# Kernel tuning notes

Hardware: AMD Instinct MI355X
Metric: run time of the kernel (lower is better)

## Reference

```python
import jax, jax.numpy as jnp
import numpy as np

LEAKY_SLOPE = 0.2

def gcn_conv(x, W, b, src, dst, deg_inv_sqrt, num_nodes):
    # GCNConv: out = D^{-1/2} (A+I) D^{-1/2} X W + b
    h = x @ W                                   # [N, out]
    norm = deg_inv_sqrt[src] * deg_inv_sqrt[dst]  # [E']
    msg = h[src] * norm[:, None]                # gather + scale
    out = jax.ops.segment_sum(msg, dst, num_segments=num_nodes)
    return out + b

def gcn_forward(x, edge_index, W1, b1, W2, b2, W3, b3):
    num_nodes = x.shape[0]
    loop = jnp.arange(num_nodes, dtype=edge_index.dtype)
    src = jnp.concatenate([edge_index[0], loop])  # add self-loops
    dst = jnp.concatenate([edge_index[1], loop])
    deg = jax.ops.segment_sum(jnp.ones_like(dst, dtype=x.dtype), dst,
                              num_segments=num_nodes)
    deg_inv_sqrt = jnp.where(deg > 0, jax.lax.rsqrt(deg), 0.0)
    # dropout is identity in eval mode (training=False)
    h = gcn_conv(x, W1, b1, src, dst, deg_inv_sqrt, num_nodes)
    h = jax.nn.leaky_relu(h, negative_slope=LEAKY_SLOPE)
    h = gcn_conv(h, W2, b2, src, dst, deg_inv_sqrt, num_nodes)
    h = jax.nn.leaky_relu(h, negative_slope=LEAKY_SLOPE)
    h = gcn_conv(h, W3, b3, src, dst, deg_inv_sqrt, num_nodes)
    return h

def setup_inputs() -> dict:
    key = jax.random.key(0)
    ks = jax.random.split(key, 8)
    N, F, E, C = 100000, 256, 3200000, 40
    x = jax.random.normal(ks[0], (N, F), dtype=jnp.float32)
    edge_index = jax.random.randint(ks[1], (2, E), 0, N, dtype=jnp.int64)
    W1 = jax.random.normal(ks[2], (F, 128), dtype=jnp.float32) * (1.0 / np.sqrt(F))
    b1 = jnp.zeros((128,), dtype=jnp.float32)
    W2 = jax.random.normal(ks[3], (128, 16), dtype=jnp.float32) * (1.0 / np.sqrt(128))
    b2 = jnp.zeros((16,), dtype=jnp.float32)
    W3 = jax.random.normal(ks[4], (16, C), dtype=jnp.float32) * (1.0 / np.sqrt(16))
    b3 = jnp.zeros((C,), dtype=jnp.float32)
    return {"x": x, "edge_index": edge_index, "W1": W1, "b1": b1,
            "W2": W2, "b2": b2, "W3": W3, "b3": b3}

def reference(x, edge_index, W1, b1, W2, b2, W3, b3):
    return gcn_forward(x, edge_index, W1, b1, W2, b2, W3, b3)
```

## Files before the change

### kernel.cpp

```cpp
#include <hip/hip_runtime.h>
#include <hip/hip_fp16.h>
#include <math.h>

#define LEAKY 0.2f
#define BP 6
#define BSZ 64
#define NBUK_MAX 2048

typedef _Float16 f16x8 __attribute__((ext_vector_type(8)));
typedef float f32x4 __attribute__((ext_vector_type(4)));

union H2 { __half2 h; int i; };
union H8 { __half2 h[4]; float4 f; };

__device__ inline __half2 shfl_xor_h2(__half2 v, int m) {
    H2 u; u.h = v;
    u.i = __shfl_xor(u.i, m);
    return u.h;
}


__global__ __launch_bounds__(256) void khist(const int* __restrict__ dst,
                                             int* __restrict__ bhist,
                                             int E, int nbuk) {
    __shared__ int hist[NBUK_MAX];
    int t = threadIdx.x;
    for (int i = t; i < nbuk; i += 256) hist[i] = 0;
    __syncthreads();
    for (int e = blockIdx.x * 256 + t; e < E; e += gridDim.x * 256)
        atomicAdd(&hist[dst[e] >> BP], 1);
    __syncthreads();
    for (int i = t; i < nbuk; i += 256) {
        int v = hist[i];
        if (v) atomicAdd(&bhist[i], v);
    }
}

__global__ __launch_bounds__(1024) void bscan(const int* __restrict__ bhist,
                                              int* __restrict__ bbase,
                                              int* __restrict__ bcur, int nbuk) {
    __shared__ int s[1024];
    int t = threadIdx.x;
    int v[4]; int sum = 0;
    #pragma unroll
    for (int i = 0; i < 4; ++i) {
        int idx = t * 4 + i;
        v[i] = (idx < nbuk) ? bhist[idx] : 0;
        sum += v[i];
    }
    s[t] = sum; __syncthreads();
    for (int off = 1; off < 1024; off <<= 1) {
        int a = (t >= off) ? s[t - off] : 0;
        __syncthreads();
        s[t] += a;
        __syncthreads();
    }
    int run = (t > 0) ? s[t - 1] : 0;
    #pragma unroll
    for (int i = 0; i < 4; ++i) {
        int idx = t * 4 + i;
        if (idx < nbuk) { bbase[idx] = run; bcur[idx] = run; run += v[i]; }
    }
    if (t == 1023) bbase[nbuk] = s[1023];
}

__global__ __launch_bounds__(256) void kscatter2(const int* __restrict__ src,
                                                 const int* __restrict__ dst,
                                                 int* __restrict__ bcur,
                                                 int* __restrict__ ebuf,
                                                 int E, int nbuk, int chunk) {
    __shared__ int hist[NBUK_MAX];
    int t = threadIdx.x;
    int base = blockIdx.x * chunk;
    int end = min(base + chunk, E);
    for (int i = t; i < nbuk; i += 256) hist[i] = 0;
    __syncthreads();
    for (int e = base + t; e < end; e += 256)
        atomicAdd(&hist[dst[e] >> BP], 1);
    __syncthreads();
    for (int i = t; i < nbuk; i += 256) {
        int c = hist[i];
        hist[i] = c ? atomicAdd(&bcur[i], c) : 0;
    }
    __syncthreads();
    for (int e = base + t; e < end; e += 256) {
        int d = dst[e];
        int pos = atomicAdd(&hist[d >> BP], 1);
        ebuf[pos] = ((d & (BSZ - 1)) << 17) | src[e];
    }
}

__global__ __launch_bounds__(256) void kcount(const int* __restrict__ ebuf,
                                              const int* __restrict__ bbase,
                                              int* __restrict__ cnt,
                                              float* __restrict__ dis, int N) {
    __shared__ int h[BSZ];
    int b = blockIdx.x, t = threadIdx.x;
    if (t < BSZ) h[t] = 0;
    __syncthreads();
    int beg = bbase[b], end = bbase[b + 1];
    for (int j = beg + t; j < end; j += 256)
        atomicAdd(&h[(ebuf[j] >> 17) & (BSZ - 1)], 1);
    __syncthreads();
    if (t < BSZ) {
        int node = b * BSZ + t;
        if (node < N) {
            int c = h[t] + 1;
            cnt[node] = c;
            dis[node] = rsqrtf((float)c);
        }
    }
}

__global__ void scan_block(const int* __restrict__ cnt, int* rowptr, int* bsum, int n) {
    __shared__ int s[256];
    int t = threadIdx.x;
    int i = blockIdx.x * 256 + t;
    int v = (i < n) ? cnt[i] : 0;
    s[t] = v; __syncthreads();
    for (int off = 1; off < 256; off <<= 1) {
        int a = (t >= off) ? s[t - off] : 0;
        __syncthreads();
        s[t] += a;
        __syncthreads();
    }
    if (i < n) rowptr[i] = s[t] - v;
    if (t == 255) bsum[blockIdx.x] = s[255];
}

__global__ void scan_tops(int* bsum, int nb, int* rowptr, int n) {
    __shared__ int s[512];
    int t = threadIdx.x;
    int v = (t < nb) ? bsum[t] : 0;
    s[t] = v; __syncthreads();
    for (int off = 1; off < 512; off <<= 1) {
        int a = (t >= off) ? s[t - off] : 0;
        __syncthreads();
        s[t] += a;
        __syncthreads();
    }
    if (t < nb) bsum[t] = s[t] - v;
    if (t == 511) rowptr[n] = s[511];
}

__global__ void scan_add(int* rowptr, const int* __restrict__ bsum, int n) {
    int i = blockIdx.x * 256 + threadIdx.x;
    if (i < n) rowptr[i] += bsum[blockIdx.x];
}

__global__ __launch_bounds__(256) void kplace(const int* __restrict__ ebuf,
                                              const int* __restrict__ bbase,
                                              const int* __restrict__ rowptr,
                                              int* __restrict__ col, int N) {
    __shared__ int cur[BSZ];
    int b = blockIdx.x, t = threadIdx.x;
    if (t < BSZ) {
        int node = b * BSZ + t;
        if (node < N) {
            int r = rowptr[node];
            col[r] = node;
            cur[t] = r + 1;
        }
    }
    __syncthreads();
    int beg = bbase[b], end = bbase[b + 1];
    for (int j = beg + t; j < end; j += 256) {
        int v = ebuf[j];
        int dl = (v >> 17) & (BSZ - 1);
        int p = atomicAdd(&cur[dl], 1);
        col[p] = v & 0x1FFFF;
    }
}

__global__ __launch_bounds__(256) void wtrans(const float* __restrict__ W1,
                                              const float* __restrict__ W2,
                                              __half* __restrict__ W1t,
                                              __half* __restrict__ W2t) {
    int idx = blockIdx.x * 256 + threadIdx.x;
    if (idx < 32768) {
        int n = idx >> 8, k = idx & 255;
        W1t[idx] = __float2half(W1[k * 128 + n]);
    } else if (idx < 32768 + 2048) {
        int i = idx - 32768;
        int n = i >> 7, k = i & 127;
        W2t[i] = __float2half(W2[k * 16 + n]);
    }
}

__global__ __launch_bounds__(256) void gemm1_mfma(
        const float* __restrict__ x, const __half* __restrict__ W1t,
        const float* __restrict__ dis, __half* __restrict__ C, int M) {
    int wave = threadIdx.x >> 6;
    int lane = threadIdx.x & 63;
    int m = lane & 15, q = lane >> 4;
    int row0 = (blockIdx.x * 4 + wave) * 16;
    int arow = row0 + m;
    bool aval = arow < M;
    const float* xr = x + (size_t)arow * 256 + q * 8;
    f32x4 acc[8];
    #pragma unroll
    for (int c = 0; c < 8; ++c) acc[c] = (f32x4){0.f, 0.f, 0.f, 0.f};
    for (int k0 = 0; k0 < 256; k0 += 32) {
        f16x8 a;
        if (aval) {
            float4 v0 = *(const float4*)(xr + k0);
            float4 v1 = *(const float4*)(xr + k0 + 4);
            a[0] = (_Float16)v0.x; a[1] = (_Float16)v0.y;
            a[2] = (_Float16)v0.z; a[3] = (_Float16)v0.w;
            a[4] = (_Float16)v1.x; a[5] = (_Float16)v1.y;
            a[6] = (_Float16)v1.z; a[7] = (_Float16)v1.w;
        } else {
            #pragma unroll
            for (int i = 0; i < 8; ++i) a[i] = (_Float16)0.f;
        }
        #pragma unroll
        for (int c = 0; c < 8; ++c) {
            f16x8 b = *(const f16x8*)(W1t + (size_t)(c * 16 + m) * 256 + k0 + q * 8);
            acc[c] = __builtin_amdgcn_mfma_f32_16x16x32_f16(a, b, acc[c], 0, 0, 0);
        }
    }
    float dw[4];
    #pragma unroll
    for (int r = 0; r < 4; ++r) {
        int rr = row0 + q * 4 + r;
        dw[r] = (rr < M) ? dis[rr] : 0.f;
    }
    #pragma unroll
    for (int c = 0; c < 8; ++c) {
        #pragma unroll
        for (int r = 0; r < 4; ++r) {
            int rr = row0 + q * 4 + r;
            if (rr < M)
                C[(size_t)rr * 128 + c * 16 + m] = __float2half(acc[c][r] * dw[r]);
        }
    }
}

__global__ __launch_bounds__(256) void gemm2_mfma(
        const __half* __restrict__ A, const __half* __restrict__ W2t,
        const float* __restrict__ dis, __half* __restrict__ C, int M) {
    int wave = threadIdx.x >> 6;
    int lane = threadIdx.x & 63;
    int m = lane & 15, q = lane >> 4;
    int row0 = (blockIdx.x * 4 + wave) * 16;
    int arow = row0 + m;
    bool aval = arow < M;
    const __half* ar = A + (size_t)arow * 128 + q * 8;
    f32x4 acc = (f32x4){0.f, 0.f, 0.f, 0.f};
    #pragma unroll
    for (int k0 = 0; k0 < 128; k0 += 32) {
        f16x8 a;
        if (aval) {
            a = *(const f16x8*)(ar + k0);
        } else {
            #pragma unroll
            for (int i = 0; i < 8; ++i) a[i] = (_Float16)0.f;
        }
        f16x8 b = *(const f16x8*)(W2t + (size_t)m * 128 + k0 + q * 8);
        acc = __builtin_amdgcn_mfma_f32_16x16x32_f16(a, b, acc, 0, 0, 0);
    }
    #pragma unroll
    for (int r = 0; r < 4; ++r) {
        int rr = row0 + q * 4 + r;
        if (rr < M)
            C[(size_t)rr * 16 + m] = __float2half(acc[r] * dis[rr]);
    }
}

__global__ __launch_bounds__(256) void prop128(
        const __half* __restrict__ h, const int* __restrict__ rowptr,
        const int* __restrict__ col, const float* __restrict__ dis,
        const float* __restrict__ bias, __half* __restrict__ out, int N) {
    int n = (blockIdx.x * 256 + threadIdx.x) >> 6;
    if (n >= N) return;
    int lane = threadIdx.x & 63;
    int eo = lane >> 4;
    int q = lane & 15;
    const float4* __restrict__ h4 = (const float4*)h;
    int beg = rowptr[n], end = rowptr[n + 1];
    __half2 acc[4];
    acc[0] = acc[1] = acc[2] = acc[3] = __float2half2_rn(0.f);
    int j = beg + eo;
    for (; j + 12 < end; j += 16) {
        int s0 = col[j], s1 = col[j + 4], s2 = col[j + 8], s3 = col[j + 12];
        H8 u0, u1, u2, u3;
        u0.f = h4[(size_t)s0 * 16 + q];
        u1.f = h4[(size_t)s1 * 16 + q];
        u2.f = h4[(size_t)s2 * 16 + q];
        u3.f = h4[(size_t)s3 * 16 + q];
        #pragma unroll
        for (int i = 0; i < 4; ++i) acc[i] = __hadd2(acc[i], u0.h[i]);
        #pragma unroll
        for (int i = 0; i < 4; ++i) acc[i] = __hadd2(acc[i], u1.h[i]);
        #pragma unroll
        for (int i = 0; i < 4; ++i) acc[i] = __hadd2(acc[i], u2.h[i]);
        #pragma unroll
        for (int i = 0; i < 4; ++i) acc[i] = __hadd2(acc[i], u3.h[i]);
    }
    for (; j + 4 < end; j += 8) {
        int s0 = col[j], s1 = col[j + 4];
        H8 u0, u1;
        u0.f = h4[(size_t)s0 * 16 + q];
        u1.f = h4[(size_t)s1 * 16 + q];
        #pragma unroll
        for (int i = 0; i < 4; ++i) acc[i] = __hadd2(acc[i], u0.h[i]);
        #pragma unroll
        for (int i = 0; i < 4; ++i) acc[i] = __hadd2(acc[i], u1.h[i]);
    }
    for (; j < end; j += 4) {
        int s = col[j];
        H8 u; u.f = h4[(size_t)s * 16 + q];
        #pragma unroll
        for (int i = 0; i < 4; ++i) acc[i] = __hadd2(acc[i], u.h[i]);
    }
    #pragma unroll
    for (int i = 0; i < 4; ++i) {
        acc[i] = __hadd2(acc[i], shfl_xor_h2(acc[i], 16));
        acc[i] = __hadd2(acc[i], shfl_xor_h2(acc[i], 32));
    }
    if (eo == 0) {
        float dn = dis[n];
        const float4* b4 = (const float4*)bias;
        float4 bA = b4[q * 2];
        float4 bB = b4[q * 2 + 1];
        float2 f0 = __half22float2(acc[0]);
        float2 f1 = __half22float2(acc[1]);
        float2 f2 = __half22float2(acc[2]);
        float2 f3 = __half22float2(acc[3]);
        float o0 = fmaf(dn, f0.x, bA.x), o1 = fmaf(dn, f0.y, bA.y);
        float o2 = fmaf(dn, f1.x, bA.z), o3 = fmaf(dn, f1.y, bA.w);
        float o4 = fmaf(dn, f2.x, bB.x), o5 = fmaf(dn, f2.y, bB.y);
        float o6 = fmaf(dn, f3.x, bB.z), o7 = fmaf(dn, f3.y, bB.w);
        o0 = o0 > 0.f ? o0 : LEAKY * o0;  o1 = o1 > 0.f ? o1 : LEAKY * o1;
        o2 = o2 > 0.f ? o2 : LEAKY * o2;  o3 = o3 > 0.f ? o3 : LEAKY * o3;
        o4 = o4 > 0.f ? o4 : LEAKY * o4;  o5 = o5 > 0.f ? o5 : LEAKY * o5;
        o6 = o6 > 0.f ? o6 : LEAKY * o6;  o7 = o7 > 0.f ? o7 : LEAKY * o7;
        H8 w;
        w.h[0] = __floats2half2_rn(o0, o1);
        w.h[1] = __floats2half2_rn(o2, o3);
        w.h[2] = __floats2half2_rn(o4, o5);
        w.h[3] = __floats2half2_rn(o6, o7);
        ((float4*)out)[(size_t)n * 16 + q] = w.f;
    }
}

__global__ __launch_bounds__(256) void prop16(
        const __half* __restrict__ h, const int* __restrict__ rowptr,
        const int* __restrict__ col, const float* __restrict__ dis,
        const float* __restrict__ bias, void* __restrict__ outp,
        int N, int act, int post, int out_fp16) {
    int t = blockIdx.x * 256 + threadIdx.x;
    int n = t >> 4;
    if (n >= N) return;
    int li = threadIdx.x & 15;
    int eo = li >> 3;
    int hq = li & 7;
    const int* __restrict__ h2i = (const int*)h;
    int beg = rowptr[n], end = rowptr[n + 1];
    __half2 acc = __float2half2_rn(0.f);
    int j = beg + eo;
    for (; j + 6 < end; j += 8) {
        H2 u0, u1, u2, u3;
        u0.i = h2i[(size_t)col[j]     * 8 + hq];
        u1.i = h2i[(size_t)col[j + 2] * 8 + hq];
        u2.i = h2i[(size_t)col[j + 4] * 8 + hq];
        u3.i = h2i[(size_t)col[j + 6] * 8 + hq];
        acc = __hadd2(acc, u0.h);
        acc = __hadd2(acc, u1.h);
        acc = __hadd2(acc, u2.h);
        acc = __hadd2(acc, u3.h);
    }
    for (; j < end; j += 2) {
        H2 u; u.i = h2i[(size_t)col[j] * 8 + hq];
        acc = __hadd2(acc, u.h);
    }
    acc = __hadd2(acc, shfl_xor_h2(acc, 8));
    if (eo == 0) {
        float dn = dis[n];
        float2 f = __half22float2(acc);
        float ox = dn * f.x, oy = dn * f.y;
        if (act) {
            ox += bias[hq * 2];
            oy += bias[hq * 2 + 1];
            ox = ox > 0.f ? ox : LEAKY * ox;
            oy = oy > 0.f ? oy : LEAKY * oy;
        }
        if (post) { ox *= dn; oy *= dn; }
        if (out_fp16) {
            H2 w; w.h = __floats2half2_rn(ox, oy);
            ((int*)outp)[(size_t)n * 8 + hq] = w.i;
        } else {
            ((float2*)outp)[(size_t)n * 8 + hq] = make_float2(ox, oy);
        }
    }
}

__global__ __launch_bounds__(256) void gemm_16_40(
        const float* __restrict__ P, const float* __restrict__ W,
        const float* __restrict__ b, float* __restrict__ out, int total) {
    __shared__ float sw[16 * 40];
    __shared__ float sb[40];
    int t = threadIdx.x;
    for (int i = t; i < 640; i += 256) sw[i] = W[i];
    if (t < 40) sb[t] = b[t];
    __syncthreads();
    int idx = blockIdx.x * 256 + t;
    if (idx >= total) return;
    int n = idx / 40, c = idx % 40;
    float acc = sb[c];
    const float* pr = P + (size_t)n * 16;
    #pragma unroll
    for (int k = 0; k < 16; ++k) acc += pr[k] * sw[k * 40 + c];
    out[idx] = acc;
}


extern "C" void kernel_launch(void* const* d_in, const int* in_sizes, int n_in,
                              void* d_out, int out_size, void* d_ws, size_t ws_size,
                              hipStream_t stream) {
    const float* x  = (const float*)d_in[0];
    const int*   ei = (const int*)d_in[1];
    const float* W1 = (const float*)d_in[2];
    const float* b1 = (const float*)d_in[3];
    const float* W2 = (const float*)d_in[4];
    const float* b2 = (const float*)d_in[5];
    const float* W3 = (const float*)d_in[6];
    const float* b3 = (const float*)d_in[7];
    float* out = (float*)d_out;

    int N = in_sizes[0] / 256;
    int E = in_sizes[1] / 2;
    const int* src = ei;
    const int* dst = ei + E;
    int NBUK = (N + BSZ - 1) >> BP;

    char* w = (char*)d_ws;
    auto alloc = [&](size_t bytes) {
        char* p = w;
        w += (bytes + 255) & ~(size_t)255;
        return p;
    };
    int NB = (N + 255) / 256;
    int*    cnt     = (int*)   alloc((size_t)N * 4);
    int*    rowptr  = (int*)   alloc((size_t)(N + 1) * 4);
    int*    bsum    = (int*)   alloc((size_t)NB * 4);
    int*    bhist   = (int*)   alloc((size_t)NBUK * 4);
    int*    bbase   = (int*)   alloc((size_t)(NBUK + 1) * 4);
    int*    bcur    = (int*)   alloc((size_t)NBUK * 4);
    int*    ebuf    = (int*)   alloc((size_t)E * 4);
    int*    colx    = (int*)   alloc((size_t)(E + N) * 4);
    float*  dis     = (float*) alloc((size_t)N * 4);
    __half* W1t     = (__half*)alloc((size_t)128 * 256 * 2);
    __half* W2t     = (__half*)alloc((size_t)16 * 128 * 2);
    __half* h1h     = (__half*)alloc((size_t)N * 128 * 2);
    __half* x1h     = (__half*)alloc((size_t)N * 128 * 2);
    __half* h2h     = (__half*)alloc((size_t)N * 16 * 2);
    __half* x2h     = (__half*)alloc((size_t)N * 16 * 2);
    float*  p3      = (float*) alloc((size_t)N * 16 * 4);

    (void)hipMemsetAsync(bhist, 0, (size_t)NBUK * 4, stream);
    wtrans  <<<136, 256, 0, stream>>>(W1, W2, W1t, W2t);
    khist   <<<256, 256, 0, stream>>>(dst, bhist, E, NBUK);
    bscan   <<<1, 1024, 0, stream>>>(bhist, bbase, bcur, NBUK);
    int SC_BLOCKS = 256;
    int chunk = (E + SC_BLOCKS - 1) / SC_BLOCKS;
    kscatter2<<<SC_BLOCKS, 256, 0, stream>>>(src, dst, bcur, ebuf, E, NBUK, chunk);
    kcount  <<<NBUK, 256, 0, stream>>>(ebuf, bbase, cnt, dis, N);
    scan_block<<<NB, 256, 0, stream>>>(cnt, rowptr, bsum, N);
    scan_tops <<<1, 512, 0, stream>>>(bsum, NB, rowptr, N);
    scan_add  <<<NB, 256, 0, stream>>>(rowptr, bsum, N);
    kplace  <<<NBUK, 256, 0, stream>>>(ebuf, bbase, rowptr, colx, N);

    int gtiles = (N + 63) / 64;
    gemm1_mfma<<<gtiles, 256, 0, stream>>>(x, W1t, dis, h1h, N);
    prop128   <<<(N * 64 + 255) / 256, 256, 0, stream>>>(h1h, rowptr, colx,
                                                         dis, b1, x1h, N);
    gemm2_mfma<<<gtiles, 256, 0, stream>>>(x1h, W2t, dis, h2h, N);
    prop16    <<<(N * 16 + 255) / 256, 256, 0, stream>>>(h2h, rowptr, colx,
                                                         dis, b2, x2h, N, 1, 1, 1);
    prop16    <<<(N * 16 + 255) / 256, 256, 0, stream>>>(x2h, rowptr, colx,
                                                         dis, nullptr, p3, N, 0, 0, 0);
    gemm_16_40<<<(N * 40 + 255) / 256, 256, 0, stream>>>(p3, W3, b3, out,
                                                         N * 40);
}
```

Before: 562.4 us.

## Fuse setup kernels, per-bucket rowptr scan, fuse last propagation with output GEMM

Merges the weight transpose into the histogram kernel and replaces the three-kernel global scan with a warp scan inside each bucket. That scan derives row offsets from the bucket base plus the self-loop count. The final 16-wide propagation is fused with the 16x40 output projection using shuffles and shared weights, which drops the p3 intermediate buffer. The gather loops in prop128 and prop16 are unrolled further to keep more loads in flight. Fewer launches and less intermediate traffic are traded for higher register use and a more specialised kernel.

```diff
diff --git a/kernel.cpp b/kernel.cpp
--- a/kernel.cpp
+++ b/kernel.cpp
@@ -19,20 +19,35 @@
     return u.h;
 }
 
-
-__global__ __launch_bounds__(256) void khist(const int* __restrict__ dst,
+__global__ __launch_bounds__(256) void kinit(const int* __restrict__ dst,
                                              int* __restrict__ bhist,
-                                             int E, int nbuk) {
-    __shared__ int hist[NBUK_MAX];
-    int t = threadIdx.x;
-    for (int i = t; i < nbuk; i += 256) hist[i] = 0;
-    __syncthreads();
-    for (int e = blockIdx.x * 256 + t; e < E; e += gridDim.x * 256)
-        atomicAdd(&hist[dst[e] >> BP], 1);
-    __syncthreads();
-    for (int i = t; i < nbuk; i += 256) {
-        int v = hist[i];
-        if (v) atomicAdd(&bhist[i], v);
+                                             int E, int nbuk,
+                                             const float* __restrict__ W1,
+                                             const float* __restrict__ W2,
+                                             __half* __restrict__ W1t,
+                                             __half* __restrict__ W2t) {
+    if (blockIdx.x < 256) {
+        __shared__ int hist[NBUK_MAX];
+        int t = threadIdx.x;
+        for (int i = t; i < nbuk; i += 256) hist[i] = 0;
+        __syncthreads();
+        for (int e = blockIdx.x * 256 + t; e < E; e += 65536)
+            atomicAdd(&hist[dst[e] >> BP], 1);
+        __syncthreads();
+        for (int i = t; i < nbuk; i += 256) {
+            int v = hist[i];
+            if (v) atomicAdd(&bhist[i], v);
+        }
+    } else {
+        int idx = (blockIdx.x - 256) * 256 + threadIdx.x;
+        if (idx < 32768) {
+            int n = idx >> 8, k = idx & 255;
+            W1t[idx] = __float2half(W1[k * 128 + n]);
+        } else if (idx < 32768 + 2048) {
+            int i = idx - 32768;
+            int n = i >> 7, k = i & 127;
+            W2t[i] = __float2half(W2[k * 16 + n]);
+        }
     }
 }
 
@@ -90,10 +105,10 @@
     }
 }
 
-__global__ __launch_bounds__(256) void kcount(const int* __restrict__ ebuf,
-                                              const int* __restrict__ bbase,
-                                              int* __restrict__ cnt,
-                                              float* __restrict__ dis, int N) {
+__global__ __launch_bounds__(256) void kcount_scan(const int* __restrict__ ebuf,
+                                                   const int* __restrict__ bbase,
+                                                   int* __restrict__ rowptr,
+                                                   float* __restrict__ dis, int N) {
     __shared__ int h[BSZ];
     int b = blockIdx.x, t = threadIdx.x;
     if (t < BSZ) h[t] = 0;
@@ -104,48 +119,20 @@
     __syncthreads();
     if (t < BSZ) {
         int node = b * BSZ + t;
+        int c = (node < N) ? h[t] + 1 : 0;
+        int incl = c;
+        #pragma unroll
+        for (int off = 1; off < 64; off <<= 1) {
+            int v = __shfl_up(incl, off);
+            if (t >= off) incl += v;
+        }
+        int colbase = beg + b * BSZ;
         if (node < N) {
-            int c = h[t] + 1;
-            cnt[node] = c;
+            rowptr[node] = colbase + incl - c;
             dis[node] = rsqrtf((float)c);
-        }
-    }
-}
-
-__global__ void scan_block(const int* __restrict__ cnt, int* rowptr, int* bsum, int n) {
-    __shared__ int s[256];
-    int t = threadIdx.x;
-    int i = blockIdx.x * 256 + t;
-    int v = (i < n) ? cnt[i] : 0;
-    s[t] = v; __syncthreads();
-    for (int off = 1; off < 256; off <<= 1) {
-        int a = (t >= off) ? s[t - off] : 0;
-        __syncthreads();
-        s[t] += a;
-        __syncthreads();
-    }
-    if (i < n) rowptr[i] = s[t] - v;
-    if (t == 255) bsum[blockIdx.x] = s[255];
-}
-
-__global__ void scan_tops(int* bsum, int nb, int* rowptr, int n) {
-    __shared__ int s[512];
-    int t = threadIdx.x;
-    int v = (t < nb) ? bsum[t] : 0;
-    s[t] = v; __syncthreads();
-    for (int off = 1; off < 512; off <<= 1) {
-        int a = (t >= off) ? s[t - off] : 0;
-        __syncthreads();
-        s[t] += a;
-        __syncthreads();
-    }
-    if (t < nb) bsum[t] = s[t] - v;
-    if (t == 511) rowptr[n] = s[511];
-}
-
-__global__ void scan_add(int* rowptr, const int* __restrict__ bsum, int n) {
-    int i = blockIdx.x * 256 + threadIdx.x;
-    if (i < n) rowptr[i] += bsum[blockIdx.x];
+            if (node == N - 1) rowptr[N] = colbase + incl;
+        }
+    }
 }
 
 __global__ __launch_bounds__(256) void kplace(const int* __restrict__ ebuf,
@@ -169,21 +156,6 @@
         int dl = (v >> 17) & (BSZ - 1);
         int p = atomicAdd(&cur[dl], 1);
         col[p] = v & 0x1FFFF;
-    }
-}
-
-__global__ __launch_bounds__(256) void wtrans(const float* __restrict__ W1,
-                                              const float* __restrict__ W2,
-                                              __half* __restrict__ W1t,
-                                              __half* __restrict__ W2t) {
-    int idx = blockIdx.x * 256 + threadIdx.x;
-    if (idx < 32768) {
-        int n = idx >> 8, k = idx & 255;
-        W1t[idx] = __float2half(W1[k * 128 + n]);
-    } else if (idx < 32768 + 2048) {
-        int i = idx - 32768;
-        int n = i >> 7, k = i & 127;
-        W2t[i] = __float2half(W2[k * 16 + n]);
     }
 }
 
@@ -281,6 +253,35 @@
     __half2 acc[4];
     acc[0] = acc[1] = acc[2] = acc[3] = __float2half2_rn(0.f);
     int j = beg + eo;
+    for (; j + 28 < end; j += 32) {
+        int s0 = col[j],      s1 = col[j + 4],  s2 = col[j + 8],  s3 = col[j + 12];
+        int s4 = col[j + 16], s5 = col[j + 20], s6 = col[j + 24], s7 = col[j + 28];
+        H8 u0, u1, u2, u3, u4, u5, u6, u7;
+        u0.f = h4[(size_t)s0 * 16 + q];
+        u1.f = h4[(size_t)s1 * 16 + q];
+        u2.f = h4[(size_t)s2 * 16 + q];
+        u3.f = h4[(size_t)s3 * 16 + q];
+        u4.f = h4[(size_t)s4 * 16 + q];
+        u5.f = h4[(size_t)s5 * 16 + q];
+        u6.f = h4[(size_t)s6 * 16 + q];
+        u7.f = h4[(size_t)s7 * 16 + q];
+        #pragma unroll
+        for (int i = 0; i < 4; ++i) acc[i] = __hadd2(acc[i], u0.h[i]);
+        #pragma unroll
+        for (int i = 0; i < 4; ++i) acc[i] = __hadd2(acc[i], u1.h[i]);
+        #pragma unroll
+        for (int i = 0; i < 4; ++i) acc[i] = __hadd2(acc[i], u2.h[i]);
+        #pragma unroll
+        for (int i = 0; i < 4; ++i) acc[i] = __hadd2(acc[i], u3.h[i]);
+        #pragma unroll
+        for (int i = 0; i < 4; ++i) acc[i] = __hadd2(acc[i], u4.h[i]);
+        #pragma unroll
+        for (int i = 0; i < 4; ++i) acc[i] = __hadd2(acc[i], u5.h[i]);
+        #pragma unroll
+        for (int i = 0; i < 4; ++i) acc[i] = __hadd2(acc[i], u6.h[i]);
+        #pragma unroll
+        for (int i = 0; i < 4; ++i) acc[i] = __hadd2(acc[i], u7.h[i]);
+    }
     for (; j + 12 < end; j += 16) {
         int s0 = col[j], s1 = col[j + 4], s2 = col[j + 8], s3 = col[j + 12];
         H8 u0, u1, u2, u3;
@@ -347,8 +348,7 @@
 __global__ __launch_bounds__(256) void prop16(
         const __half* __restrict__ h, const int* __restrict__ rowptr,
         const int* __restrict__ col, const float* __restrict__ dis,
-        const float* __restrict__ bias, void* __restrict__ outp,
-        int N, int act, int post, int out_fp16) {
+        const float* __restrict__ bias, __half* __restrict__ outp, int N) {
     int t = blockIdx.x * 256 + threadIdx.x;
     int n = t >> 4;
     if (n >= N) return;
@@ -359,16 +359,29 @@
     int beg = rowptr[n], end = rowptr[n + 1];
     __half2 acc = __float2half2_rn(0.f);
     int j = beg + eo;
+    for (; j + 14 < end; j += 16) {
+        H2 u0, u1, u2, u3, u4, u5, u6, u7;
+        u0.i = h2i[(size_t)col[j]      * 8 + hq];
+        u1.i = h2i[(size_t)col[j + 2]  * 8 + hq];
+        u2.i = h2i[(size_t)col[j + 4]  * 8 + hq];
+        u3.i = h2i[(size_t)col[j + 6]  * 8 + hq];
+        u4.i = h2i[(size_t)col[j + 8]  * 8 + hq];
+        u5.i = h2i[(size_t)col[j + 10] * 8 + hq];
+        u6.i = h2i[(size_t)col[j + 12] * 8 + hq];
+        u7.i = h2i[(size_t)col[j + 14] * 8 + hq];
+        acc = __hadd2(acc, u0.h); acc = __hadd2(acc, u1.h);
+        acc = __hadd2(acc, u2.h); acc = __hadd2(acc, u3.h);
+        acc = __hadd2(acc, u4.h); acc = __hadd2(acc, u5.h);
+        acc = __hadd2(acc, u6.h); acc = __hadd2(acc, u7.h);
+    }
     for (; j + 6 < end; j += 8) {
         H2 u0, u1, u2, u3;
         u0.i = h2i[(size_t)col[j]     * 8 + hq];
         u1.i = h2i[(size_t)col[j + 2] * 8 + hq];
         u2.i = h2i[(size_t)col[j + 4] * 8 + hq];
         u3.i = h2i[(size_t)col[j + 6] * 8 + hq];
-        acc = __hadd2(acc, u0.h);
-        acc = __hadd2(acc, u1.h);
-        acc = __hadd2(acc, u2.h);
-        acc = __hadd2(acc, u3.h);
+        acc = __hadd2(acc, u0.h); acc = __hadd2(acc, u1.h);
+        acc = __hadd2(acc, u2.h); acc = __hadd2(acc, u3.h);
     }
     for (; j < end; j += 2) {
         H2 u; u.i = h2i[(size_t)col[j] * 8 + hq];
@@ -378,40 +391,89 @@
     if (eo == 0) {
         float dn = dis[n];
         float2 f = __half22float2(acc);
-        float ox = dn * f.x, oy = dn * f.y;
-        if (act) {
-            ox += bias[hq * 2];
-            oy += bias[hq * 2 + 1];
-            ox = ox > 0.f ? ox : LEAKY * ox;
-            oy = oy > 0.f ? oy : LEAKY * oy;
-        }
-        if (post) { ox *= dn; oy *= dn; }
-        if (out_fp16) {
-            H2 w; w.h = __floats2half2_rn(ox, oy);
-            ((int*)outp)[(size_t)n * 8 + hq] = w.i;
-        } else {
-            ((float2*)outp)[(size_t)n * 8 + hq] = make_float2(ox, oy);
-        }
-    }
-}
-
-__global__ __launch_bounds__(256) void gemm_16_40(
-        const float* __restrict__ P, const float* __restrict__ W,
-        const float* __restrict__ b, float* __restrict__ out, int total) {
-    __shared__ float sw[16 * 40];
+        float ox = fmaf(dn, f.x, bias[hq * 2]);
+        float oy = fmaf(dn, f.y, bias[hq * 2 + 1]);
+        ox = ox > 0.f ? ox : LEAKY * ox;
+        oy = oy > 0.f ? oy : LEAKY * oy;
+        ox *= dn; oy *= dn;
+        H2 w; w.h = __floats2half2_rn(ox, oy);
+        ((int*)outp)[(size_t)n * 8 + hq] = w.i;
+    }
+}
+
+__global__ __launch_bounds__(256) void prop16_gemm3(
+        const __half* __restrict__ h, const int* __restrict__ rowptr,
+        const int* __restrict__ col, const float* __restrict__ dis,
+        const float* __restrict__ W3, const float* __restrict__ b3,
+        float* __restrict__ out, int N) {
+    __shared__ float sw[640];
     __shared__ float sb[40];
-    int t = threadIdx.x;
-    for (int i = t; i < 640; i += 256) sw[i] = W[i];
-    if (t < 40) sb[t] = b[t];
-    __syncthreads();
-    int idx = blockIdx.x * 256 + t;
-    if (idx >= total) return;
-    int n = idx / 40, c = idx % 40;
-    float acc = sb[c];
-    const float* pr = P + (size_t)n * 16;
-    #pragma unroll
-    for (int k = 0; k < 16; ++k) acc += pr[k] * sw[k * 40 + c];
-    out[idx] = acc;
+    int t0 = threadIdx.x;
+    for (int i = t0; i < 640; i += 256) sw[i] = W3[i];
+    if (t0 < 40) sb[t0] = b3[t0];
+    __syncthreads();
+    int t = blockIdx.x * 256 + t0;
+    int n = t >> 4;
+    if (n >= N) return;
+    int li = t0 & 15;
+    int eo = li >> 3;
+    int hq = li & 7;
+    const int* __restrict__ h2i = (const int*)h;
+    int beg = rowptr[n], end = rowptr[n + 1];
+    __half2 acc = __float2half2_rn(0.f);
+    int j = beg + eo;
+    for (; j + 14 < end; j += 16) {
+        H2 u0, u1, u2, u3, u4, u5, u6, u7;
+        u0.i = h2i[(size_t)col[j]      * 8 + hq];
+        u1.i = h2i[(size_t)col[j + 2]  * 8 + hq];
+        u2.i = h2i[(size_t)col[j + 4]  * 8 + hq];
+        u3.i = h2i[(size_t)col[j + 6]  * 8 + hq];
+        u4.i = h2i[(size_t)col[j + 8]  * 8 + hq];
+        u5.i = h2i[(size_t)col[j + 10] * 8 + hq];
+        u6.i = h2i[(size_t)col[j + 12] * 8 + hq];
+        u7.i = h2i[(size_t)col[j + 14] * 8 + hq];
+        acc = __hadd2(acc, u0.h); acc = __hadd2(acc, u1.h);
+        acc = __hadd2(acc, u2.h); acc = __hadd2(acc, u3.h);
+        acc = __hadd2(acc, u4.h); acc = __hadd2(acc, u5.h);
+        acc = __hadd2(acc, u6.h); acc = __hadd2(acc, u7.h);
+    }
+    for (; j + 6 < end; j += 8) {
+        H2 u0, u1, u2, u3;
+        u0.i = h2i[(size_t)col[j]     * 8 + hq];
+        u1.i = h2i[(size_t)col[j + 2] * 8 + hq];
+        u2.i = h2i[(size_t)col[j + 4] * 8 + hq];
+        u3.i = h2i[(size_t)col[j + 6] * 8 + hq];
+        acc = __hadd2(acc, u0.h); acc = __hadd2(acc, u1.h);
+        acc = __hadd2(acc, u2.h); acc = __hadd2(acc, u3.h);
+    }
+    for (; j < end; j += 2) {
+        H2 u; u.i = h2i[(size_t)col[j] * 8 + hq];
+        acc = __hadd2(acc, u.h);
+    }
+    acc = __hadd2(acc, shfl_xor_h2(acc, 8));
+    float dn = dis[n];
+    int slot = (t0 & 63) & ~15;
+    H2 av; av.h = acc;
+    float oA = 0.f, oB = 0.f, oC = 0.f;
+    #pragma unroll
+    for (int hh = 0; hh < 8; ++hh) {
+        H2 u; u.i = __shfl(av.i, slot + hh);
+        float2 p = __half22float2(u.h);
+        float p0 = dn * p.x, p1 = dn * p.y;
+        int k0 = hh * 2;
+        oA = fmaf(p0, sw[k0 * 40 + li],            oA);
+        oA = fmaf(p1, sw[(k0 + 1) * 40 + li],      oA);
+        oB = fmaf(p0, sw[k0 * 40 + li + 16],       oB);
+        oB = fmaf(p1, sw[(k0 + 1) * 40 + li + 16], oB);
+        if (li < 8) {
+            oC = fmaf(p0, sw[k0 * 40 + li + 32],       oC);
+            oC = fmaf(p1, sw[(k0 + 1) * 40 + li + 32], oC);
+        }
+    }
+    float* orow = out + (size_t)n * 40;
+    orow[li]      = oA + sb[li];
+    orow[li + 16] = oB + sb[li + 16];
+    if (li < 8) orow[li + 32] = oC + sb[li + 32];
 }
 
 
@@ -440,10 +502,7 @@
         w += (bytes + 255) & ~(size_t)255;
         return p;
     };
-    int NB = (N + 255) / 256;
-    int*    cnt     = (int*)   alloc((size_t)N * 4);
     int*    rowptr  = (int*)   alloc((size_t)(N + 1) * 4);
-    int*    bsum    = (int*)   alloc((size_t)NB * 4);
     int*    bhist   = (int*)   alloc((size_t)NBUK * 4);
     int*    bbase   = (int*)   alloc((size_t)(NBUK + 1) * 4);
     int*    bcur    = (int*)   alloc((size_t)NBUK * 4);
@@ -456,19 +515,14 @@
     __half* x1h     = (__half*)alloc((size_t)N * 128 * 2);
     __half* h2h     = (__half*)alloc((size_t)N * 16 * 2);
     __half* x2h     = (__half*)alloc((size_t)N * 16 * 2);
-    float*  p3      = (float*) alloc((size_t)N * 16 * 4);
 
     (void)hipMemsetAsync(bhist, 0, (size_t)NBUK * 4, stream);
-    wtrans  <<<136, 256, 0, stream>>>(W1, W2, W1t, W2t);
-    khist   <<<256, 256, 0, stream>>>(dst, bhist, E, NBUK);
+    kinit   <<<392, 256, 0, stream>>>(dst, bhist, E, NBUK, W1, W2, W1t, W2t);
     bscan   <<<1, 1024, 0, stream>>>(bhist, bbase, bcur, NBUK);
     int SC_BLOCKS = 256;
     int chunk = (E + SC_BLOCKS - 1) / SC_BLOCKS;
     kscatter2<<<SC_BLOCKS, 256, 0, stream>>>(src, dst, bcur, ebuf, E, NBUK, chunk);
-    kcount  <<<NBUK, 256, 0, stream>>>(ebuf, bbase, cnt, dis, N);
-    scan_block<<<NB, 256, 0, stream>>>(cnt, rowptr, bsum, N);
-    scan_tops <<<1, 512, 0, stream>>>(bsum, NB, rowptr, N);
-    scan_add  <<<NB, 256, 0, stream>>>(rowptr, bsum, N);
+    kcount_scan<<<NBUK, 256, 0, stream>>>(ebuf, bbase, rowptr, dis, N);
     kplace  <<<NBUK, 256, 0, stream>>>(ebuf, bbase, rowptr, colx, N);
 
     int gtiles = (N + 63) / 64;
@@ -477,9 +531,7 @@
                                                          dis, b1, x1h, N);
     gemm2_mfma<<<gtiles, 256, 0, stream>>>(x1h, W2t, dis, h2h, N);
     prop16    <<<(N * 16 + 255) / 256, 256, 0, stream>>>(h2h, rowptr, colx,
-                                                         dis, b2, x2h, N, 1, 1, 1);
-    prop16    <<<(N * 16 + 255) / 256, 256, 0, stream>>>(x2h, rowptr, colx,
-                                                         dis, nullptr, p3, N, 0, 0, 0);
-    gemm_16_40<<<(N * 40 + 255) / 256, 256, 0, stream>>>(p3, W3, b3, out,
-                                                         N * 40);
-}
+                                                         dis, b2, x2h, N);
+    prop16_gemm3<<<(N * 16 + 255) / 256, 256, 0, stream>>>(x2h, rowptr, colx,
+                                                           dis, W3, b3, out, N);
+}
```

Measured after the change: 535.1 us. 4.8% less time.
